# Optimization experiments

Hardware: AMD Instinct MI355X
Metric: run time of the kernel (lower is better)

Reference implementation:

```python
import jax, jax.numpy as jnp
import numpy as np

B, N, D, S, H, ITERS = 64, 4096, 128, 7, 256, 3
EPS = 1e-8

def layer_norm(x, g, b):
    m = jnp.mean(x, axis=-1, keepdims=True)
    v = jnp.var(x, axis=-1, keepdims=True)
    return (x - m) * jax.lax.rsqrt(v + 1e-5) * g + b

def setup_inputs() -> dict:
    key = jax.random.key(0)
    ks = jax.random.split(key, 16)
    lin = lambda k, o, i: jax.random.normal(k, (o, i), jnp.float32) / np.sqrt(i)
    return {
        "embeddings": jax.random.normal(ks[0], (B, N, D), jnp.float32),
        "noise": jax.random.normal(ks[1], (B, S, D), jnp.float32),
        "slots_mu": jax.random.normal(ks[2], (1, 1, D), jnp.float32),
        "slots_sigma": jax.random.uniform(ks[3], (1, 1, D), jnp.float32),
        "Wk": lin(ks[4], D, D), "bk": jnp.zeros((D,), jnp.float32),
        "Wq": lin(ks[5], D, D), "bq": jnp.zeros((D,), jnp.float32),
        "Wv": lin(ks[6], D, D), "bv": jnp.zeros((D,), jnp.float32),
        "W_ih": lin(ks[7], 3 * D, D), "W_hh": lin(ks[8], 3 * D, D),
        "b_ih": jnp.zeros((3 * D,), jnp.float32), "b_hh": jnp.zeros((3 * D,), jnp.float32),
        "W1": lin(ks[9], H, D), "b1": jnp.zeros((H,), jnp.float32),
        "W2": lin(ks[10], D, H), "b2": jnp.zeros((D,), jnp.float32),
        "ln_in_g": jnp.ones((D,), jnp.float32), "ln_in_b": jnp.zeros((D,), jnp.float32),
        "ln_s_g": jnp.ones((D,), jnp.float32), "ln_s_b": jnp.zeros((D,), jnp.float32),
        "ln_ff_g": jnp.ones((D,), jnp.float32), "ln_ff_b": jnp.zeros((D,), jnp.float32),
    }

def reference(embeddings, noise, slots_mu, slots_sigma, Wk, bk, Wq, bq, Wv, bv,
              W_ih, W_hh, b_ih, b_hh, W1, b1, W2, b2,
              ln_in_g, ln_in_b, ln_s_g, ln_s_b, ln_ff_g, ln_ff_b):
    # slot init: normal(mu, sigma) with fixed noise
    slots = slots_mu + slots_sigma * noise  # [B,S,D]
    emb = layer_norm(embeddings, ln_in_g, ln_in_b)
    keys = emb @ Wk.T + bk      # [B,N,D]
    values = emb @ Wv.T + bv    # [B,N,D]
    for _ in range(ITERS):
        slots_prev = slots
        q = layer_norm(slots, ln_s_g, ln_s_b) @ Wq.T + bq  # [B,S,D]
        dots = jnp.einsum('bid,bjd->bij', q, keys)          # [B,S,N]
        attn = jax.nn.softmax(dots, axis=-1) + EPS
        attn = attn / jnp.sum(attn, axis=-1, keepdims=True)
        updates = jnp.einsum('bjd,bij->bid', values, attn)  # [B,S,D]
        # GRUCell (pytorch gate order: r, z, n)
        x = updates.reshape(-1, D)
        h = slots_prev.reshape(-1, D)
        gi = x @ W_ih.T + b_ih
        gh = h @ W_hh.T + b_hh
        gi_r, gi_z, gi_n = jnp.split(gi, 3, axis=-1)
        gh_r, gh_z, gh_n = jnp.split(gh, 3, axis=-1)
        r = jax.nn.sigmoid(gi_r + gh_r)
        z = jax.nn.sigmoid(gi_z + gh_z)
        n = jnp.tanh(gi_n + r * gh_n)
        slots = ((1.0 - z) * n + z * h).reshape(B, S, D)
        ff = jax.nn.relu(layer_norm(slots, ln_ff_g, ln_ff_b) @ W1.T + b1) @ W2.T + b2
        slots = slots + ff
    return slots
```

## Files before the change

### kernel.cpp

```cpp
#include <hip/hip_runtime.h>
#include <math.h>

#define B_ 64
#define N_ 4096
#define D_ 128
#define S_ 7
#define H_ 256
#define ITERS_ 3
#define AP 132
#define NCHUNK 16

__device__ __forceinline__ float dot4(float4 a, float4 b) {
  return a.x * b.x + a.y * b.y + a.z * b.z + a.w * b.w;
}
__device__ __forceinline__ float4 ld4(const float* p) {
  return *reinterpret_cast<const float4*>(p);
}

__global__ void k_init(const float* __restrict__ noise, const float* __restrict__ mu,
                       const float* __restrict__ sigma, float* __restrict__ slots) {
  int idx = blockIdx.x * 256 + threadIdx.x;
  int d = idx & 127;
  slots[idx] = mu[d] + sigma[d] * noise[idx];
}

__global__ __launch_bounds__(128) void k_q(
    const float* __restrict__ slots, const float* __restrict__ Wq, const float* __restrict__ bq,
    const float* __restrict__ g, const float* __restrict__ b,
    const float* __restrict__ Wk, float* __restrict__ qp) {
  __shared__ __align__(16) float lns[AP];
  __shared__ __align__(16) float qs2[AP];
  __shared__ float red[4];
  int row = blockIdx.x;
  int d = threadIdx.x;
  float x = slots[row * D_ + d];
  float s1 = x, s2 = x * x;
#pragma unroll
  for (int off = 32; off >= 1; off >>= 1) { s1 += __shfl_down(s1, off); s2 += __shfl_down(s2, off); }
  if ((d & 63) == 0) { red[(d >> 6) * 2] = s1; red[(d >> 6) * 2 + 1] = s2; }
  __syncthreads();
  float sum = red[0] + red[2], sumsq = red[1] + red[3];
  float mean = sum * (1.f / 128.f);
  float var = sumsq * (1.f / 128.f) - mean * mean;
  float rs = rsqrtf(var + 1e-5f);
  lns[d] = (x - mean) * rs * g[d] + b[d];
  __syncthreads();
  const float* w = Wq + d * D_;
  float acc = bq[d];
  for (int i4 = 0; i4 < D_; i4 += 4) acc += dot4(*reinterpret_cast<const float4*>(&lns[i4]), ld4(w + i4));
  qs2[d] = acc;
  __syncthreads();
  float qpa = 0.f;
#pragma unroll 4
  for (int dd = 0; dd < D_; dd++) qpa += qs2[dd] * Wk[dd * D_ + d];
  qp[row * D_ + d] = qpa;
}

__global__ __launch_bounds__(256) void k_attn(
    const float* __restrict__ qpbuf, const float* __restrict__ emb,
    const float* __restrict__ lng, const float* __restrict__ lnb,
    float* __restrict__ partialA, float* __restrict__ partialM, float* __restrict__ partialS) {
  __shared__ __align__(16) float qs[7 * AP];
  __shared__ __align__(16) float vt[64 * AP];
  __shared__ float red[28 * 64];
  __shared__ float pt[7 * 64];
  __shared__ float sm[7], ssum[7], tmax[7];
  int t = threadIdx.x;
  int b = blockIdx.x >> 4, jc = blockIdx.x & (NCHUNK - 1);

  if (t < 224) {
    int s = t >> 5, i4 = (t & 31) * 4;
    *reinterpret_cast<float4*>(&qs[s * AP + i4]) = ld4(&qpbuf[(b * 7 + s) * D_ + i4]);
  }
  if (t < 7) { sm[t] = -1e30f; ssum[t] = 0.f; }

  int j = t & 63, g = t >> 6, ib = g * 32;
  int d4 = (t & 31) * 4, jg = t >> 5;
  int ln_i4 = (t & 31) * 4;
  int ln_r8 = t >> 5;
  float4 gv = ld4(&lng[ln_i4]);
  float4 bv4 = ld4(&lnb[ln_i4]);

  float acc[7][4];
#pragma unroll
  for (int s = 0; s < 7; s++)
#pragma unroll
    for (int c = 0; c < 4; c++) acc[s][c] = 0.f;
  __syncthreads();

  for (int sub = 0; sub < 4; sub++) {
    int j0 = jc * 256 + sub * 64;
#pragma unroll
    for (int u = 0; u < 8; u++) {
      int row = u * 8 + ln_r8;
      float4 x = ld4(&emb[((long)b * N_ + j0 + row) * D_ + ln_i4]);
      float s1 = x.x + x.y + x.z + x.w;
      float s2 = dot4(x, x);
#pragma unroll
      for (int off = 16; off >= 1; off >>= 1) {
        s1 += __shfl_xor(s1, off, 32);
        s2 += __shfl_xor(s2, off, 32);
      }
      float mean = s1 * (1.f / 128.f);
      float var = s2 * (1.f / 128.f) - mean * mean;
      float rs = rsqrtf(var + 1e-5f);
      float4 o;
      o.x = (x.x - mean) * rs * gv.x + bv4.x;
      o.y = (x.y - mean) * rs * gv.y + bv4.y;
      o.z = (x.z - mean) * rs * gv.z + bv4.z;
      o.w = (x.w - mean) * rs * gv.w + bv4.w;
      *reinterpret_cast<float4*>(&vt[row * AP + ln_i4]) = o;
    }
    __syncthreads();

    float acc7[7];
#pragma unroll
    for (int s = 0; s < 7; s++) acc7[s] = 0.f;
#pragma unroll
    for (int st = 0; st < 8; st++) {
      float4 kv = *reinterpret_cast<const float4*>(&vt[j * AP + ib + st * 4]);
#pragma unroll
      for (int s = 0; s < 7; s++) {
        float4 qv = *reinterpret_cast<const float4*>(&qs[s * AP + ib + st * 4]);
        acc7[s] += dot4(kv, qv);
      }
    }
#pragma unroll
    for (int s = 0; s < 7; s++) red[(g * 7 + s) * 64 + j] = acc7[s];
    __syncthreads();

    for (int pp = t; pp < 448; pp += 256) {
      int s = pp >> 6, jj = pp & 63;
      pt[pp] = red[s * 64 + jj] + red[(7 + s) * 64 + jj] +
               red[(14 + s) * 64 + jj] + red[(21 + s) * 64 + jj];
    }
    __syncthreads();

    if (t < 224) {
      int s = t >> 5, i = t & 31;
      float m = fmaxf(pt[s * 64 + i], pt[s * 64 + 32 + i]);
#pragma unroll
      for (int off = 16; off >= 1; off >>= 1) m = fmaxf(m, __shfl_down(m, off, 32));
      if ((t & 31) == 0) tmax[s] = m;
    }
    __syncthreads();

#pragma unroll
    for (int s = 0; s < 7; s++) {
      float mnew = fmaxf(sm[s], tmax[s]);
      float scl = __expf(sm[s] - mnew);
#pragma unroll
      for (int c = 0; c < 4; c++) acc[s][c] *= scl;
    }
    for (int pp = t; pp < 448; pp += 256) {
      int s = pp >> 6;
      float mnew = fmaxf(sm[s], tmax[s]);
      pt[pp] = __expf(pt[pp] - mnew);
    }
    __syncthreads();

    if (t < 224) {
      int s = t >> 5, i = t & 31;
      float ssub = pt[s * 64 + i] + pt[s * 64 + 32 + i];
#pragma unroll
      for (int off = 16; off >= 1; off >>= 1) ssub += __shfl_down(ssub, off, 32);
      if ((t & 31) == 0) {
        float mnew = fmaxf(sm[s], tmax[s]);
        float scl = __expf(sm[s] - mnew);
        ssum[s] = ssum[s] * scl + ssub;
        sm[s] = mnew;
      }
    }

#pragma unroll
    for (int jl = 0; jl < 8; jl++) {
      int jj = jg * 8 + jl;
      float4 vv = *reinterpret_cast<const float4*>(&vt[jj * AP + d4]);
#pragma unroll
      for (int s = 0; s < 7; s++) {
        float e = pt[s * 64 + jj];
        acc[s][0] += e * vv.x; acc[s][1] += e * vv.y;
        acc[s][2] += e * vv.z; acc[s][3] += e * vv.w;
      }
    }
    __syncthreads();
  }

  float* redf = vt;
#pragma unroll
  for (int s = 0; s < 7; s++)
    *reinterpret_cast<float4*>(&redf[(jg * 7 + s) * 128 + d4]) =
        make_float4(acc[s][0], acc[s][1], acc[s][2], acc[s][3]);
  __syncthreads();
  for (int pp = t; pp < 896; pp += 256) {
    int s = pp >> 7, d = pp & 127;
    float x = 0.f;
#pragma unroll
    for (int g2 = 0; g2 < 8; g2++) x += redf[(g2 * 7 + s) * 128 + d];
    partialA[((long)(b * NCHUNK + jc) * 7 + s) * 128 + d] = x;
  }
  if (t < 7) {
    partialM[(b * NCHUNK + jc) * 7 + t] = sm[t];
    partialS[(b * NCHUNK + jc) * 7 + t] = ssum[t];
  }
}

__global__ __launch_bounds__(128) void k_gruff(
    const float* __restrict__ partialA, const float* __restrict__ partialM,
    const float* __restrict__ partialS, float* __restrict__ slots,
    const float* __restrict__ Wv, const float* __restrict__ bv,
    const float* __restrict__ Wih, const float* __restrict__ Whh,
    const float* __restrict__ bih, const float* __restrict__ bhh,
    const float* __restrict__ W1, const float* __restrict__ b1,
    const float* __restrict__ W2, const float* __restrict__ b2,
    const float* __restrict__ gff, const float* __restrict__ bff) {
  __shared__ __align__(16) float us[AP];
  __shared__ __align__(16) float xs[AP];
  __shared__ __align__(16) float hs[AP];
  __shared__ __align__(16) float lns[AP];
  __shared__ __align__(16) float h1s[H_];
  __shared__ float red4[4];
  int blk = blockIdx.x;
  int b = blk / 7, s = blk % 7;
  int d = threadIdx.x;

  float mg = -1e30f;
#pragma unroll
  for (int c = 0; c < NCHUNK; c++) mg = fmaxf(mg, partialM[(b * NCHUNK + c) * 7 + s]);
  float denom = 0.f, up = 0.f;
#pragma unroll
  for (int c = 0; c < NCHUNK; c++) {
    float w = __expf(partialM[(b * NCHUNK + c) * 7 + s] - mg);
    denom += w * partialS[(b * NCHUNK + c) * 7 + s];
    up += w * partialA[((long)(b * NCHUNK + c) * 7 + s) * 128 + d];
  }
  us[d] = up / denom;
  __syncthreads();

  float x = bv[d];
  {
    const float* wvr = Wv + d * D_;
    for (int i4 = 0; i4 < D_; i4 += 4)
      x += dot4(*reinterpret_cast<const float4*>(&us[i4]), ld4(wvr + i4));
  }
  float h = slots[blk * D_ + d];
  xs[d] = x; hs[d] = h;
  __syncthreads();

  float gir = bih[d], giz = bih[128 + d], gin = bih[256 + d];
  float ghr = bhh[d], ghz = bhh[128 + d], ghn = bhh[256 + d];
  const float* wir = Wih + d * D_;
  const float* wiz = Wih + (128 + d) * D_;
  const float* win = Wih + (256 + d) * D_;
  const float* whr = Whh + d * D_;
  const float* whz = Whh + (128 + d) * D_;
  const float* whn = Whh + (256 + d) * D_;
  for (int i4 = 0; i4 < D_; i4 += 4) {
    float4 xv = *reinterpret_cast<const float4*>(&xs[i4]);
    float4 hv = *reinterpret_cast<const float4*>(&hs[i4]);
    gir += dot4(xv, ld4(wir + i4)); giz += dot4(xv, ld4(wiz + i4)); gin += dot4(xv, ld4(win + i4));
    ghr += dot4(hv, ld4(whr + i4)); ghz += dot4(hv, ld4(whz + i4)); ghn += dot4(hv, ld4(whn + i4));
  }
  float r = 1.f / (1.f + __expf(-(gir + ghr)));
  float z = 1.f / (1.f + __expf(-(giz + ghz)));
  float n = tanhf(gin + r * ghn);
  float ns = (1.f - z) * n + z * h;

  float s1 = ns, s2 = ns * ns;
#pragma unroll
  for (int off = 32; off >= 1; off >>= 1) { s1 += __shfl_down(s1, off); s2 += __shfl_down(s2, off); }
  if ((d & 63) == 0) { red4[(d >> 6) * 2] = s1; red4[(d >> 6) * 2 + 1] = s2; }
  __syncthreads();
  float sum = red4[0] + red4[2], sumsq = red4[1] + red4[3];
  float mean = sum * (1.f / 128.f);
  float var = sumsq * (1.f / 128.f) - mean * mean;
  float rs = rsqrtf(var + 1e-5f);
  lns[d] = (ns - mean) * rs * gff[d] + bff[d];
  __syncthreads();

  float a0 = b1[d], a1 = b1[d + 128];
  const float* w1a = W1 + d * D_;
  const float* w1b = W1 + (128 + d) * D_;
  for (int i4 = 0; i4 < D_; i4 += 4) {
    float4 lv = *reinterpret_cast<const float4*>(&lns[i4]);
    a0 += dot4(lv, ld4(w1a + i4));
    a1 += dot4(lv, ld4(w1b + i4));
  }
  h1s[d] = fmaxf(a0, 0.f);
  h1s[d + 128] = fmaxf(a1, 0.f);
  __syncthreads();

  float f = b2[d];
  const float* w2r = W2 + d * H_;
  for (int h4 = 0; h4 < H_; h4 += 4)
    f += dot4(*reinterpret_cast<const float4*>(&h1s[h4]), ld4(w2r + h4));
  slots[blk * D_ + d] = ns + f;
}

extern "C" void kernel_launch(void* const* d_in, const int* in_sizes, int n_in,
                              void* d_out, int out_size, void* d_ws, size_t ws_size,
                              hipStream_t stream) {
  const float* emb   = (const float*)d_in[0];
  const float* noise = (const float*)d_in[1];
  const float* mu    = (const float*)d_in[2];
  const float* sigma = (const float*)d_in[3];
  const float* Wk = (const float*)d_in[4];  const float* bk = (const float*)d_in[5];
  const float* Wq = (const float*)d_in[6];  const float* bq = (const float*)d_in[7];
  const float* Wv = (const float*)d_in[8];  const float* bv = (const float*)d_in[9];
  const float* Wih = (const float*)d_in[10]; const float* Whh = (const float*)d_in[11];
  const float* bih = (const float*)d_in[12]; const float* bhh = (const float*)d_in[13];
  const float* W1 = (const float*)d_in[14];  const float* b1 = (const float*)d_in[15];
  const float* W2 = (const float*)d_in[16];  const float* b2 = (const float*)d_in[17];
  const float* lin_g = (const float*)d_in[18]; const float* lin_b = (const float*)d_in[19];
  const float* ls_g  = (const float*)d_in[20]; const float* ls_b  = (const float*)d_in[21];
  const float* lff_g = (const float*)d_in[22]; const float* lff_b = (const float*)d_in[23];
  (void)bk;

  float* slots = (float*)d_out;
  float* qp       = (float*)d_ws;
  float* partialA = qp + (size_t)B_ * S_ * D_;
  float* partialM = partialA + (size_t)B_ * NCHUNK * S_ * D_;
  float* partialS = partialM + (size_t)B_ * NCHUNK * S_;

  k_init<<<224, 256, 0, stream>>>(noise, mu, sigma, slots);
  for (int it = 0; it < ITERS_; it++) {
    k_q<<<448, 128, 0, stream>>>(slots, Wq, bq, ls_g, ls_b, Wk, qp);
    k_attn<<<B_ * NCHUNK, 256, 0, stream>>>(qp, emb, lin_g, lin_b, partialA, partialM, partialS);
    k_gruff<<<448, 128, 0, stream>>>(partialA, partialM, partialS, slots, Wv, bv,
                                     Wih, Whh, bih, bhh, W1, b1, W2, b2, lff_g, lff_b);
  }
}
```

Baseline: 545.5 us.

## Fuse next-iteration query projection into GRU kernel, widen it, halve attention chunks

The per-iteration query kernel is folded into the tail of the GRU/FF kernel, so each slot block produces the projected query for the next iteration and two launches are removed. The GRU kernel grows to 256 threads, splitting the matvecs (Wv, Wih vs Whh, W1 rows, W2 halves, Wq, Wk) across two halves with shared-memory reductions. Attention now uses 8 chunks of 512 keys instead of 16 of 256, which halves the partial buffers but leaves only 512 attention blocks, lowering parallelism across the GPU.

After: 537.2 us. About the same (-1.5%).

```diff
diff --git a/kernel.cpp b/kernel.cpp
--- a/kernel.cpp
+++ b/kernel.cpp
@@ -8,7 +8,7 @@
 #define H_ 256
 #define ITERS_ 3
 #define AP 132
-#define NCHUNK 16
+#define NCHUNK 8
 
 __device__ __forceinline__ float dot4(float4 a, float4 b) {
   return a.x * b.x + a.y * b.y + a.z * b.z + a.w * b.w;
@@ -66,7 +66,7 @@
   __shared__ float pt[7 * 64];
   __shared__ float sm[7], ssum[7], tmax[7];
   int t = threadIdx.x;
-  int b = blockIdx.x >> 4, jc = blockIdx.x & (NCHUNK - 1);
+  int b = blockIdx.x >> 3, jc = blockIdx.x & (NCHUNK - 1);
 
   if (t < 224) {
     int s = t >> 5, i4 = (t & 31) * 4;
@@ -88,8 +88,8 @@
     for (int c = 0; c < 4; c++) acc[s][c] = 0.f;
   __syncthreads();
 
-  for (int sub = 0; sub < 4; sub++) {
-    int j0 = jc * 256 + sub * 64;
+  for (int sub = 0; sub < 8; sub++) {
+    int j0 = jc * 512 + sub * 64;
 #pragma unroll
     for (int u = 0; u < 8; u++) {
       int row = u * 8 + ln_r8;
@@ -205,7 +205,7 @@
   }
 }
 
-__global__ __launch_bounds__(128) void k_gruff(
+__global__ __launch_bounds__(256) void k_gruffq(
     const float* __restrict__ partialA, const float* __restrict__ partialM,
     const float* __restrict__ partialS, float* __restrict__ slots,
     const float* __restrict__ Wv, const float* __restrict__ bv,
@@ -213,88 +213,161 @@
     const float* __restrict__ bih, const float* __restrict__ bhh,
     const float* __restrict__ W1, const float* __restrict__ b1,
     const float* __restrict__ W2, const float* __restrict__ b2,
-    const float* __restrict__ gff, const float* __restrict__ bff) {
+    const float* __restrict__ gff, const float* __restrict__ bff,
+    const float* __restrict__ lsg, const float* __restrict__ lsb,
+    const float* __restrict__ Wq, const float* __restrict__ bq,
+    const float* __restrict__ Wk, float* __restrict__ qp, int compute_q) {
   __shared__ __align__(16) float us[AP];
   __shared__ __align__(16) float xs[AP];
   __shared__ __align__(16) float hs[AP];
+  __shared__ __align__(16) float nss[AP];
   __shared__ __align__(16) float lns[AP];
+  __shared__ __align__(16) float sn[AP];
+  __shared__ __align__(16) float qv[AP];
   __shared__ __align__(16) float h1s[H_];
-  __shared__ float red4[4];
+  __shared__ __align__(16) float g6[6 * 128];
+  __shared__ __align__(16) float pp[2 * 128];
+  __shared__ float den2[2];
+  __shared__ float red2[2];
+  int t = threadIdx.x;
+  int d = t & 127, h = t >> 7;
   int blk = blockIdx.x;
   int b = blk / 7, s = blk % 7;
-  int d = threadIdx.x;
 
   float mg = -1e30f;
 #pragma unroll
   for (int c = 0; c < NCHUNK; c++) mg = fmaxf(mg, partialM[(b * NCHUNK + c) * 7 + s]);
-  float denom = 0.f, up = 0.f;
-#pragma unroll
-  for (int c = 0; c < NCHUNK; c++) {
+  float up = 0.f, den = 0.f;
+#pragma unroll
+  for (int cc = 0; cc < NCHUNK / 2; cc++) {
+    int c = h * (NCHUNK / 2) + cc;
     float w = __expf(partialM[(b * NCHUNK + c) * 7 + s] - mg);
-    denom += w * partialS[(b * NCHUNK + c) * 7 + s];
+    den += w * partialS[(b * NCHUNK + c) * 7 + s];
     up += w * partialA[((long)(b * NCHUNK + c) * 7 + s) * 128 + d];
   }
-  us[d] = up / denom;
-  __syncthreads();
-
-  float x = bv[d];
-  {
-    const float* wvr = Wv + d * D_;
+  pp[h * 128 + d] = up;
+  if (d == 0) den2[h] = den;
+  if (h == 1) hs[d] = slots[blk * D_ + d];
+  __syncthreads();
+  if (h == 0) us[d] = (pp[d] + pp[128 + d]) / (den2[0] + den2[1]);
+  __syncthreads();
+
+  {
+    const float* wvr = Wv + d * D_ + h * 64;
+    float acc = 0.f;
+    for (int i4 = 0; i4 < 64; i4 += 4)
+      acc += dot4(*reinterpret_cast<const float4*>(&us[h * 64 + i4]), ld4(wvr + i4));
+    pp[h * 128 + d] = acc;
+  }
+  __syncthreads();
+  if (h == 0) xs[d] = bv[d] + pp[d] + pp[128 + d];
+  __syncthreads();
+
+  {
+    const float* base = (h == 0) ? Wih : Whh;
+    const float* bias = (h == 0) ? bih : bhh;
+    const float* vec = (h == 0) ? xs : hs;
+    float a0 = bias[d], a1 = bias[128 + d], a2 = bias[256 + d];
+    const float* w0 = base + d * D_;
+    const float* w1 = base + (128 + d) * D_;
+    const float* w2 = base + (256 + d) * D_;
+    for (int i4 = 0; i4 < D_; i4 += 4) {
+      float4 v = *reinterpret_cast<const float4*>(&vec[i4]);
+      a0 += dot4(v, ld4(w0 + i4));
+      a1 += dot4(v, ld4(w1 + i4));
+      a2 += dot4(v, ld4(w2 + i4));
+    }
+    g6[(h * 3 + 0) * 128 + d] = a0;
+    g6[(h * 3 + 1) * 128 + d] = a1;
+    g6[(h * 3 + 2) * 128 + d] = a2;
+  }
+  __syncthreads();
+  if (h == 0) {
+    float gir = g6[d], giz = g6[128 + d], gin = g6[256 + d];
+    float ghr = g6[384 + d], ghz = g6[512 + d], ghn = g6[640 + d];
+    float r = 1.f / (1.f + __expf(-(gir + ghr)));
+    float z = 1.f / (1.f + __expf(-(giz + ghz)));
+    float n = tanhf(gin + r * ghn);
+    nss[d] = (1.f - z) * n + z * hs[d];
+  }
+  __syncthreads();
+
+  if (t < 64) {
+    float v0 = nss[t], v1 = nss[t + 64];
+    float s1 = v0 + v1, s2 = v0 * v0 + v1 * v1;
+#pragma unroll
+    for (int off = 32; off >= 1; off >>= 1) { s1 += __shfl_down(s1, off); s2 += __shfl_down(s2, off); }
+    if (t == 0) { red2[0] = s1; red2[1] = s2; }
+  }
+  __syncthreads();
+  {
+    float mean = red2[0] * (1.f / 128.f);
+    float var = red2[1] * (1.f / 128.f) - mean * mean;
+    float rs = rsqrtf(var + 1e-5f);
+    if (h == 0) lns[d] = (nss[d] - mean) * rs * gff[d] + bff[d];
+  }
+  __syncthreads();
+
+  {
+    float a = b1[t];
+    const float* w = W1 + t * D_;
     for (int i4 = 0; i4 < D_; i4 += 4)
-      x += dot4(*reinterpret_cast<const float4*>(&us[i4]), ld4(wvr + i4));
-  }
-  float h = slots[blk * D_ + d];
-  xs[d] = x; hs[d] = h;
-  __syncthreads();
-
-  float gir = bih[d], giz = bih[128 + d], gin = bih[256 + d];
-  float ghr = bhh[d], ghz = bhh[128 + d], ghn = bhh[256 + d];
-  const float* wir = Wih + d * D_;
-  const float* wiz = Wih + (128 + d) * D_;
-  const float* win = Wih + (256 + d) * D_;
-  const float* whr = Whh + d * D_;
-  const float* whz = Whh + (128 + d) * D_;
-  const float* whn = Whh + (256 + d) * D_;
-  for (int i4 = 0; i4 < D_; i4 += 4) {
-    float4 xv = *reinterpret_cast<const float4*>(&xs[i4]);
-    float4 hv = *reinterpret_cast<const float4*>(&hs[i4]);
-    gir += dot4(xv, ld4(wir + i4)); giz += dot4(xv, ld4(wiz + i4)); gin += dot4(xv, ld4(win + i4));
-    ghr += dot4(hv, ld4(whr + i4)); ghz += dot4(hv, ld4(whz + i4)); ghn += dot4(hv, ld4(whn + i4));
-  }
-  float r = 1.f / (1.f + __expf(-(gir + ghr)));
-  float z = 1.f / (1.f + __expf(-(giz + ghz)));
-  float n = tanhf(gin + r * ghn);
-  float ns = (1.f - z) * n + z * h;
-
-  float s1 = ns, s2 = ns * ns;
-#pragma unroll
-  for (int off = 32; off >= 1; off >>= 1) { s1 += __shfl_down(s1, off); s2 += __shfl_down(s2, off); }
-  if ((d & 63) == 0) { red4[(d >> 6) * 2] = s1; red4[(d >> 6) * 2 + 1] = s2; }
-  __syncthreads();
-  float sum = red4[0] + red4[2], sumsq = red4[1] + red4[3];
-  float mean = sum * (1.f / 128.f);
-  float var = sumsq * (1.f / 128.f) - mean * mean;
-  float rs = rsqrtf(var + 1e-5f);
-  lns[d] = (ns - mean) * rs * gff[d] + bff[d];
-  __syncthreads();
-
-  float a0 = b1[d], a1 = b1[d + 128];
-  const float* w1a = W1 + d * D_;
-  const float* w1b = W1 + (128 + d) * D_;
-  for (int i4 = 0; i4 < D_; i4 += 4) {
-    float4 lv = *reinterpret_cast<const float4*>(&lns[i4]);
-    a0 += dot4(lv, ld4(w1a + i4));
-    a1 += dot4(lv, ld4(w1b + i4));
-  }
-  h1s[d] = fmaxf(a0, 0.f);
-  h1s[d + 128] = fmaxf(a1, 0.f);
-  __syncthreads();
-
-  float f = b2[d];
-  const float* w2r = W2 + d * H_;
-  for (int h4 = 0; h4 < H_; h4 += 4)
-    f += dot4(*reinterpret_cast<const float4*>(&h1s[h4]), ld4(w2r + h4));
-  slots[blk * D_ + d] = ns + f;
+      a += dot4(*reinterpret_cast<const float4*>(&lns[i4]), ld4(w + i4));
+    h1s[t] = fmaxf(a, 0.f);
+  }
+  __syncthreads();
+
+  {
+    const float* w2r = W2 + d * H_ + h * 128;
+    float acc = 0.f;
+    for (int h4 = 0; h4 < 128; h4 += 4)
+      acc += dot4(*reinterpret_cast<const float4*>(&h1s[h * 128 + h4]), ld4(w2r + h4));
+    pp[h * 128 + d] = acc;
+  }
+  __syncthreads();
+  if (h == 0) {
+    float out = nss[d] + b2[d] + pp[d] + pp[128 + d];
+    sn[d] = out;
+    slots[blk * D_ + d] = out;
+  }
+  __syncthreads();
+
+  if (!compute_q) return;
+
+  if (t < 64) {
+    float v0 = sn[t], v1 = sn[t + 64];
+    float s1 = v0 + v1, s2 = v0 * v0 + v1 * v1;
+#pragma unroll
+    for (int off = 32; off >= 1; off >>= 1) { s1 += __shfl_down(s1, off); s2 += __shfl_down(s2, off); }
+    if (t == 0) { red2[0] = s1; red2[1] = s2; }
+  }
+  __syncthreads();
+  {
+    float mean = red2[0] * (1.f / 128.f);
+    float var = red2[1] * (1.f / 128.f) - mean * mean;
+    float rs = rsqrtf(var + 1e-5f);
+    if (h == 0) lns[d] = (sn[d] - mean) * rs * lsg[d] + lsb[d];
+  }
+  __syncthreads();
+  {
+    const float* w = Wq + d * D_ + h * 64;
+    float acc = 0.f;
+    for (int i4 = 0; i4 < 64; i4 += 4)
+      acc += dot4(*reinterpret_cast<const float4*>(&lns[h * 64 + i4]), ld4(w + i4));
+    pp[h * 128 + d] = acc;
+  }
+  __syncthreads();
+  if (h == 0) qv[d] = bq[d] + pp[d] + pp[128 + d];
+  __syncthreads();
+  {
+    float acc = 0.f;
+    const float* wc = Wk + h * 64 * D_ + d;
+#pragma unroll 4
+    for (int dd = 0; dd < 64; dd++) acc += qv[h * 64 + dd] * wc[dd * D_];
+    pp[h * 128 + d] = acc;
+  }
+  __syncthreads();
+  if (h == 0) qp[blk * D_ + d] = pp[d] + pp[128 + d];
 }
 
 extern "C" void kernel_launch(void* const* d_in, const int* in_sizes, int n_in,
@@ -323,10 +396,11 @@
   float* partialS = partialM + (size_t)B_ * NCHUNK * S_;
 
   k_init<<<224, 256, 0, stream>>>(noise, mu, sigma, slots);
+  k_q<<<448, 128, 0, stream>>>(slots, Wq, bq, ls_g, ls_b, Wk, qp);
   for (int it = 0; it < ITERS_; it++) {
-    k_q<<<448, 128, 0, stream>>>(slots, Wq, bq, ls_g, ls_b, Wk, qp);
     k_attn<<<B_ * NCHUNK, 256, 0, stream>>>(qp, emb, lin_g, lin_b, partialA, partialM, partialS);
-    k_gruff<<<448, 128, 0, stream>>>(partialA, partialM, partialS, slots, Wv, bv,
-                                     Wih, Whh, bih, bhh, W1, b1, W2, b2, lff_g, lff_b);
-  }
-}
+    k_gruffq<<<448, 256, 0, stream>>>(partialA, partialM, partialS, slots, Wv, bv,
+                                      Wih, Whh, bih, bhh, W1, b1, W2, b2, lff_g, lff_b,
+                                      ls_g, ls_b, Wq, bq, Wk, qp, it < ITERS_ - 1 ? 1 : 0);
+  }
+}
```
